# Kernel optimization log

Measured on AMD Instinct MI355X. Metric: run time of the kernel, lower is better.

## Reference

```python
import jax, jax.numpy as jnp
import numpy as np

N_NODES = 100000
N_EDGES = 1600000
IN_DIM = 160
HID = 128
BN_EPS = 1e-5


def setup_inputs() -> dict:
    key = jax.random.key(0)
    ks = jax.random.split(key, 16)
    d = {}
    d['x'] = jax.random.normal(ks[0], (N_NODES, IN_DIM), dtype=jnp.float32)
    d['edge_index'] = jax.random.randint(ks[1], (2, N_EDGES), 0, N_NODES, dtype=jnp.int64)
    dims = [(IN_DIM, HID), (HID, HID), (HID, HID)]
    for i, (fi, fo) in enumerate(dims):
        s = 1.0 / np.sqrt(fi)
        d[f'wl{i}'] = jax.random.normal(ks[2 + 4 * i], (fi, fo), dtype=jnp.float32) * s
        d[f'wr{i}'] = jax.random.normal(ks[3 + 4 * i], (fi, fo), dtype=jnp.float32) * s
        d[f'bl{i}'] = jnp.zeros((fo,), dtype=jnp.float32)
        d[f'g{i}'] = jnp.ones((fo,), dtype=jnp.float32)
        d[f'be{i}'] = jnp.zeros((fo,), dtype=jnp.float32)
        d[f'rm{i}'] = jax.random.normal(ks[4 + 4 * i], (fo,), dtype=jnp.float32) * 0.1
        d[f'rv{i}'] = jnp.ones((fo,), dtype=jnp.float32)
    d['lin_w'] = jax.random.normal(ks[14], (HID, 1), dtype=jnp.float32) * (1.0 / np.sqrt(HID))
    d['lin_b'] = jnp.zeros((1,), dtype=jnp.float32)
    return d


def _sage_bn_relu(h, src, dst, wl, wr, bl, g, be, rm, rv):
    # mean neighbor aggregation: gather messages at src, scatter-mean to dst
    msg = h[src]                                            # [E, d]
    agg = jax.ops.segment_sum(msg, dst, num_segments=N_NODES)
    cnt = jax.ops.segment_sum(jnp.ones((msg.shape[0],), h.dtype), dst, num_segments=N_NODES)
    mean = agg / jnp.maximum(cnt, 1.0)[:, None]             # nodes w/o in-edges -> 0
    out = mean @ wl + bl + h @ wr                           # SAGEConv (root_weight=True)
    # BatchNorm1d (inference: running stats) + ReLU
    out = (out - rm) * (g * jax.lax.rsqrt(rv + BN_EPS)) + be
    return jax.nn.relu(out)


def reference(x, edge_index,
              wl0, wr0, bl0, g0, be0, rm0, rv0,
              wl1, wr1, bl1, g1, be1, rm1, rv1,
              wl2, wr2, bl2, g2, be2, rm2, rv2,
              lin_w, lin_b):
    src, dst = edge_index[0], edge_index[1]
    h = _sage_bn_relu(x, src, dst, wl0, wr0, bl0, g0, be0, rm0, rv0)
    h = _sage_bn_relu(h, src, dst, wl1, wr1, bl1, g1, be1, rm1, rv1)
    h = _sage_bn_relu(h, src, dst, wl2, wr2, bl2, g2, be2, rm2, rv2)
    return (h @ lin_w + lin_b)[:, 0]                        # [N]
```

## Files before the change

### kernel.cpp

```cpp
#include <hip/hip_runtime.h>

#define N_NODES 100000
#define N_EDGES 1600000
#define IN_DIM 160
#define HID 128
#define BN_EPS 1e-5f

#define M_PAD 100096
#define NBUCK 196
#define BSH 9
#define EPB 8192
#define NHB (NBUCK * NBUCK)
#define NSB 38
#define LPAD 132

typedef unsigned int uint;
typedef unsigned short ushort;
typedef __attribute__((ext_vector_type(8))) short bf16x8;
typedef __attribute__((ext_vector_type(4))) float f32x4;
typedef __attribute__((ext_vector_type(2))) float f32x2;

__device__ __forceinline__ ushort bf16rn(float f) {
    uint u = __float_as_uint(f);
    u += 0x7fffu + ((u >> 16) & 1u);
    return (ushort)(u >> 16);
}
__device__ __forceinline__ float bflo(uint u) { return __uint_as_float(u << 16); }
__device__ __forceinline__ float bfhi(uint u) { return __uint_as_float(u & 0xffff0000u); }


__global__ __launch_bounds__(256) void hist_kernel(const int* __restrict__ dst,
                                                   int* __restrict__ ghist) {
    __shared__ int hist[NBUCK];
    int b = blockIdx.x, t = threadIdx.x;
    for (int i = t; i < NBUCK; i += 256) hist[i] = 0;
    __syncthreads();
    int e0 = b * EPB;
    for (int i = 0; i < EPB; i += 256) {
        int e = e0 + i + t;
        if (e < N_EDGES) atomicAdd(&hist[dst[e] >> BSH], 1);
    }
    __syncthreads();
    for (int i = t; i < NBUCK; i += 256) ghist[i * NBUCK + b] = hist[i];
}

__global__ __launch_bounds__(256) void scan1_kernel(const int* __restrict__ ghist,
                                                    int* __restrict__ bsum) {
    __shared__ int wsum[4];
    int b = blockIdx.x, t = threadIdx.x;
    int i4 = b * 256 + t;
    int4 v = (i4 * 4 < NHB) ? ((const int4*)ghist)[i4] : make_int4(0, 0, 0, 0);
    int s = v.x + v.y + v.z + v.w;
#pragma unroll
    for (int off = 32; off; off >>= 1) s += __shfl_down(s, off);
    if ((t & 63) == 0) wsum[t >> 6] = s;
    __syncthreads();
    if (t == 0) bsum[b] = wsum[0] + wsum[1] + wsum[2] + wsum[3];
}

__global__ void scan2_kernel(const int* __restrict__ bsum, int* __restrict__ boff,
                             int* __restrict__ gbb) {
    int lane = threadIdx.x;
    int v = (lane < NSB) ? bsum[lane] : 0;
    int s = v;
#pragma unroll
    for (int off = 1; off <= 32; off <<= 1) {
        int t2 = __shfl_up(s, off);
        if (lane >= off) s += t2;
    }
    if (lane < NSB) boff[lane] = s - v;
    if (lane == 0) gbb[NBUCK] = N_EDGES;
}

__global__ __launch_bounds__(256) void scan3_kernel(int* __restrict__ ghist,
                                                    const int* __restrict__ boff,
                                                    int* __restrict__ gbb) {
    __shared__ int ts[256];
    int b = blockIdx.x, t = threadIdx.x;
    int i4 = b * 256 + t;
    bool ok = (i4 * 4) < NHB;
    int4 v = ok ? ((const int4*)ghist)[i4] : make_int4(0, 0, 0, 0);
    int s = v.x + v.y + v.z + v.w;
    ts[t] = s;
    __syncthreads();
    for (int off = 1; off < 256; off <<= 1) {
        int a = (t >= off) ? ts[t - off] : 0;
        __syncthreads();
        ts[t] += a;
        __syncthreads();
    }
    int excl = boff[b] + ((t > 0) ? ts[t - 1] : 0);
    if (ok) {
        int idx = i4 * 4;
        int4 w;
        w.x = excl;
        w.y = excl + v.x;
        w.z = excl + v.x + v.y;
        w.w = excl + v.x + v.y + v.z;
        ((int4*)ghist)[i4] = w;
        if (idx % NBUCK == 0) gbb[idx / NBUCK] = w.x;
    }
}

__global__ __launch_bounds__(256) void scatter_kernel(const int* __restrict__ src,
                                                      const int* __restrict__ dst,
                                                      const int* __restrict__ ghist,
                                                      uint* __restrict__ scat) {
    __shared__ int base[NBUCK];
    __shared__ int fill[NBUCK];
    int b = blockIdx.x, t = threadIdx.x;
    for (int i = t; i < NBUCK; i += 256) { base[i] = ghist[i * NBUCK + b]; fill[i] = 0; }
    __syncthreads();
    int e0 = b * EPB;
    for (int i = 0; i < EPB; i += 256) {
        int e = e0 + i + t;
        if (e < N_EDGES) {
            int d = dst[e];
            int sv = src[e];
            int bk = d >> BSH;
            int lp = atomicAdd(&fill[bk], 1);
            scat[base[bk] + lp] = (uint)sv | ((uint)(d & 511) << 17);
        }
    }
}

__global__ __launch_bounds__(256) void bucket_csr_kernel(const uint* __restrict__ scat,
                                                         const int* __restrict__ gbb,
                                                         int* __restrict__ prow,
                                                         int* __restrict__ deg,
                                                         int* __restrict__ peidx) {
    __shared__ int cnt[512], fl[512], pref[512];
    __shared__ int ts[256];
    __shared__ int tot_s;
    int b = blockIdx.x, t = threadIdx.x;
    int beg = gbb[b], end = gbb[b + 1];
    int pb = beg + b * 8192;
    cnt[t] = 0; cnt[t + 256] = 0;
    __syncthreads();
    for (int i = beg + t; i < end; i += 256)
        atomicAdd(&cnt[scat[i] >> 17], 1);
    __syncthreads();
    int c0 = cnt[2 * t], c1 = cnt[2 * t + 1];
    int p0 = (c0 + 15) & ~15, p1 = (c1 + 15) & ~15;
    ts[t] = p0 + p1;
    __syncthreads();
    for (int off = 1; off < 256; off <<= 1) {
        int v = (t >= off) ? ts[t - off] : 0;
        __syncthreads();
        ts[t] += v;
        __syncthreads();
    }
    int ex = (t > 0) ? ts[t - 1] : 0;
    pref[2 * t] = ex;
    pref[2 * t + 1] = ex + p0;
    fl[t] = 0; fl[t + 256] = 0;
    if (t == 255) tot_s = ts[255];
    int g0 = b * 512 + 2 * t;
    if (g0 < N_NODES) { prow[g0] = pb + ex; deg[g0] = c0; }
    if (g0 + 1 < N_NODES) { prow[g0 + 1] = pb + ex + p0; deg[g0 + 1] = c1; }
    __syncthreads();
    int tot = tot_s;
    for (int i = t; i < tot; i += 256) peidx[pb + i] = N_NODES;
    __syncthreads();
    for (int i = beg + t; i < end; i += 256) {
        uint w = scat[i];
        int nl = (int)(w >> 17);
        int lp = atomicAdd(&fl[nl], 1);
        peidx[pb + pref[nl] + lp] = (int)(w & 0x1FFFFu);
    }
}

__global__ void prep_weights_kernel(const float* __restrict__ wl, const float* __restrict__ wr,
                                    ushort* __restrict__ Bf, int K) {
    int kb = blockIdx.x >> 4;
    int tt = blockIdx.x & 15;
    int lane = threadIdx.x;
    int n = tt * 16 + (lane & 15);
    int k0 = kb * 32 + (lane >> 4) * 8;
    ushort* dst = Bf + ((size_t)(kb * 16 + tt) * 64 + lane) * 8;
#pragma unroll
    for (int e = 0; e < 8; ++e) {
        int k = k0 + e;
        float v = (n < HID) ? wl[k * HID + n] : wr[k * HID + (n - HID)];
        dst[e] = bf16rn(v);
    }
}

__global__ void bn_prep_kernel(const float* __restrict__ bl0, const float* __restrict__ g0,
                               const float* __restrict__ be0, const float* __restrict__ rm0,
                               const float* __restrict__ rv0,
                               const float* __restrict__ bl1, const float* __restrict__ g1,
                               const float* __restrict__ be1, const float* __restrict__ rm1,
                               const float* __restrict__ rv1,
                               const float* __restrict__ bl2, const float* __restrict__ g2,
                               const float* __restrict__ be2, const float* __restrict__ rm2,
                               const float* __restrict__ rv2,
                               float* __restrict__ scale, float* __restrict__ shift) {
    int t = threadIdx.x;
    int L = t >> 7, j = t & 127;
    const float* bl = (L == 0) ? bl0 : (L == 1) ? bl1 : bl2;
    const float* g  = (L == 0) ? g0  : (L == 1) ? g1  : g2;
    const float* be = (L == 0) ? be0 : (L == 1) ? be1 : be2;
    const float* rm = (L == 0) ? rm0 : (L == 1) ? rm1 : rm2;
    const float* rv = (L == 0) ? rv0 : (L == 1) ? rv1 : rv2;
    float s = g[j] * rsqrtf(rv[j] + BN_EPS);
    scale[t] = s;
    shift[t] = (bl[j] - rm[j]) * s + be[j];
}

template <int K, bool AFP32>
__global__ __launch_bounds__(256) void gemm_kernel(const void* __restrict__ A_,
                                                   const ushort* __restrict__ Bf,
                                                   ushort* __restrict__ tl,
                                                   ushort* __restrict__ troot) {
    constexpr int CPR = K / 8;
    constexpr int FULLG = CPR & ~7;
    constexpr int LDSE = (64 * K > 4 * 16 * LPAD) ? 64 * K : 4 * 16 * LPAD;
    __shared__ ushort ldsA[LDSE];
    const int t = threadIdx.x;
    const int m0b = blockIdx.x * 64;

#pragma unroll
    for (int i = 0; i < (64 * CPR) / 256; ++i) {
        int cidx = i * 256 + t;
        int row = cidx / CPR;
        int j = cidx - row * CPR;
        bf16x8 v;
        if (AFP32) {
            const float* A = (const float*)A_;
            int m = m0b + row;
            float4 f0 = make_float4(0.f, 0.f, 0.f, 0.f), f1 = f0;
            if (m < N_NODES) {
                f0 = *(const float4*)(A + (size_t)m * K + j * 8);
                f1 = *(const float4*)(A + (size_t)m * K + j * 8 + 4);
            }
            v[0] = (short)bf16rn(f0.x); v[1] = (short)bf16rn(f0.y);
            v[2] = (short)bf16rn(f0.z); v[3] = (short)bf16rn(f0.w);
            v[4] = (short)bf16rn(f1.x); v[5] = (short)bf16rn(f1.y);
            v[6] = (short)bf16rn(f1.z); v[7] = (short)bf16rn(f1.w);
        } else {
            const ushort* A = (const ushort*)A_;
            v = *(const bf16x8*)(A + (size_t)(m0b + row) * K + j * 8);
        }
        int swz = (j < FULLG) ? ((j & ~7) | ((j ^ row) & 7))
                              : ((j & ~3) | ((j ^ row) & 3));
        *(bf16x8*)&ldsA[row * K + swz * 8] = v;
    }
    __syncthreads();

    const int lane = threadIdx.x & 63;
    const int wv = threadIdx.x >> 6;
    const int col = lane & 15;
    const int q = lane >> 4;
    const int rh = wv & 1;
    const int ch = wv >> 1;
    const int row0 = rh * 32 + col;
    f32x4 acc0[8], acc1[8];
#pragma unroll
    for (int tt = 0; tt < 8; ++tt) {
        acc0[tt] = (f32x4){0.f, 0.f, 0.f, 0.f};
        acc1[tt] = (f32x4){0.f, 0.f, 0.f, 0.f};
    }

#pragma unroll
    for (int kb = 0; kb < K / 32; ++kb) {
        int jj = kb * 4 + q;
        int swzj = (jj < FULLG) ? ((jj & ~7) | ((jj ^ col) & 7))
                                : ((jj & ~3) | ((jj ^ col) & 3));
        bf16x8 a0 = *(const bf16x8*)&ldsA[row0 * K + swzj * 8];
        bf16x8 a1 = *(const bf16x8*)&ldsA[(row0 + 16) * K + swzj * 8];
        const ushort* bp = Bf + ((size_t)((kb * 16 + ch * 8) * 64) + lane) * 8;
#pragma unroll
        for (int tt = 0; tt < 8; ++tt) {
            bf16x8 bfr = *(const bf16x8*)(bp + (size_t)tt * 64 * 8);
            acc0[tt] = __builtin_amdgcn_mfma_f32_16x16x32_bf16(a0, bfr, acc0[tt], 0, 0, 0);
            acc1[tt] = __builtin_amdgcn_mfma_f32_16x16x32_bf16(a1, bfr, acc1[tt], 0, 0, 0);
        }
    }

    __syncthreads();
    ushort(*rp)[16][LPAD] = (ushort(*)[16][LPAD])ldsA;
    ushort* outp = ch ? troot : tl;
#pragma unroll
    for (int mt = 0; mt < 2; ++mt) {
        const f32x4* ac = mt ? acc1 : acc0;
#pragma unroll
        for (int tt = 0; tt < 8; ++tt)
#pragma unroll
            for (int r = 0; r < 4; ++r)
                rp[wv][q * 4 + r][tt * 16 + col] = bf16rn(ac[tt][r]);
        int mbase = m0b + rh * 32 + mt * 16;
#pragma unroll
        for (int i = 0; i < 4; ++i) {
            int lin = i * 64 + lane;
            int row = lin >> 4;
            int c16 = lin & 15;
            bf16x8 v = *(const bf16x8*)&rp[wv][row][c16 * 8];
            *(bf16x8*)(outp + (size_t)(mbase + row) * HID + c16 * 8) = v;
        }
    }
}

template <bool FINAL>
__global__ __launch_bounds__(256) void agg_kernel(
    const ushort* __restrict__ tl_, const ushort* __restrict__ troot_,
    const int* __restrict__ prow, const int* __restrict__ deg_,
    const int* __restrict__ peidx,
    const float* __restrict__ bnscale, const float* __restrict__ bnshift,
    const float* __restrict__ linw, const float* __restrict__ linb,
    ushort* __restrict__ hout, float* __restrict__ out) {
    const int lane = threadIdx.x & 63;
    const int wvg = (blockIdx.x * 256 + (int)threadIdx.x) >> 6;
    const int g = lane >> 4;
    const int s = lane & 15;
    const int n = wvg * 4 + g;
    const int nn = (n < N_NODES) ? n : (N_NODES - 1);

    float4 sc0 = *(const float4*)(bnscale + s * 8);
    float4 sc1 = *(const float4*)(bnscale + s * 8 + 4);
    float4 sh0 = *(const float4*)(bnshift + s * 8);
    float4 sh1 = *(const float4*)(bnshift + s * 8 + 4);

    int pbeg = prow[nn];
    int dg = (n < N_NODES) ? deg_[nn] : 0;
    int myb = (dg + 15) >> 4;

    f32x2 acc2[4];
#pragma unroll
    for (int i = 0; i < 4; ++i) acc2[i] = (f32x2){0.f, 0.f};

    const int gsel = (lane & 48) << 2;

    for (int b = 0;; ++b) {
        bool act = b < myb;
        if (!__any(act)) break;
        int idx = act ? peidx[pbeg + b * 16 + s] : N_NODES;
        uint4 u[16];
#pragma unroll
        for (int jj = 0; jj < 16; ++jj) {
            int src = __builtin_amdgcn_ds_bpermute(gsel | (jj << 2), idx);
            u[jj] = *(const uint4*)(tl_ + (size_t)src * HID + s * 8);
        }
#pragma unroll
        for (int jj = 0; jj < 16; ++jj) {
            acc2[0] += (f32x2){bflo(u[jj].x), bfhi(u[jj].x)};
            acc2[1] += (f32x2){bflo(u[jj].y), bfhi(u[jj].y)};
            acc2[2] += (f32x2){bflo(u[jj].z), bfhi(u[jj].z)};
            acc2[3] += (f32x2){bflo(u[jj].w), bfhi(u[jj].w)};
        }
    }

    float inv = 1.0f / (float)((dg > 0) ? dg : 1);
    uint4 rv = *(const uint4*)(troot_ + (size_t)nn * HID + s * 8);
    float o[8];
    o[0] = fmaxf(fmaf(fmaf(acc2[0].x, inv, bflo(rv.x)), sc0.x, sh0.x), 0.f);
    o[1] = fmaxf(fmaf(fmaf(acc2[0].y, inv, bfhi(rv.x)), sc0.y, sh0.y), 0.f);
    o[2] = fmaxf(fmaf(fmaf(acc2[1].x, inv, bflo(rv.y)), sc0.z, sh0.z), 0.f);
    o[3] = fmaxf(fmaf(fmaf(acc2[1].y, inv, bfhi(rv.y)), sc0.w, sh0.w), 0.f);
    o[4] = fmaxf(fmaf(fmaf(acc2[2].x, inv, bflo(rv.z)), sc1.x, sh1.x), 0.f);
    o[5] = fmaxf(fmaf(fmaf(acc2[2].y, inv, bfhi(rv.z)), sc1.y, sh1.y), 0.f);
    o[6] = fmaxf(fmaf(fmaf(acc2[3].x, inv, bflo(rv.w)), sc1.z, sh1.z), 0.f);
    o[7] = fmaxf(fmaf(fmaf(acc2[3].y, inv, bfhi(rv.w)), sc1.w, sh1.w), 0.f);

    if (FINAL) {
        float4 w0 = *(const float4*)(linw + s * 8);
        float4 w1 = *(const float4*)(linw + s * 8 + 4);
        float p = o[0] * w0.x + o[1] * w0.y + o[2] * w0.z + o[3] * w0.w +
                  o[4] * w1.x + o[5] * w1.y + o[6] * w1.z + o[7] * w1.w;
#pragma unroll
        for (int off = 1; off < 16; off <<= 1) p += __shfl_xor(p, off);
        if (s == 0 && n < N_NODES) out[n] = p + linb[0];
    } else {
        uint4 pk = make_uint4(0u, 0u, 0u, 0u);
        if (n < N_NODES) {
            pk.x = (uint)bf16rn(o[0]) | ((uint)bf16rn(o[1]) << 16);
            pk.y = (uint)bf16rn(o[2]) | ((uint)bf16rn(o[3]) << 16);
            pk.z = (uint)bf16rn(o[4]) | ((uint)bf16rn(o[5]) << 16);
            pk.w = (uint)bf16rn(o[6]) | ((uint)bf16rn(o[7]) << 16);
        }
        *(uint4*)(hout + (size_t)n * HID + s * 8) = pk;
    }
}


extern "C" void kernel_launch(void* const* d_in, const int* in_sizes, int n_in,
                              void* d_out, int out_size, void* d_ws, size_t ws_size,
                              hipStream_t stream) {
    const float* x    = (const float*)d_in[0];
    const int*   ei   = (const int*)d_in[1];
    const int*   esrc = ei;
    const int*   edst = ei + N_EDGES;
    const float* wl[3]; const float* wr[3]; const float* bl[3];
    const float* g[3];  const float* be[3]; const float* rm[3]; const float* rv[3];
    for (int i = 0; i < 3; ++i) {
        wl[i] = (const float*)d_in[2 + 7 * i];
        wr[i] = (const float*)d_in[3 + 7 * i];
        bl[i] = (const float*)d_in[4 + 7 * i];
        g[i]  = (const float*)d_in[5 + 7 * i];
        be[i] = (const float*)d_in[6 + 7 * i];
        rm[i] = (const float*)d_in[7 + 7 * i];
        rv[i] = (const float*)d_in[8 + 7 * i];
    }
    const float* lin_w = (const float*)d_in[23];
    const float* lin_b = (const float*)d_in[24];
    float* out = (float*)d_out;

    char* ws = (char*)d_ws;
    size_t off = 0;
    auto carve = [&](size_t bytes) -> void* {
        void* p = ws + off;
        off += (bytes + 255) & ~(size_t)255;
        return p;
    };
    int*    prow   = (int*)carve((size_t)(N_NODES + 8) * sizeof(int));
    int*    deg    = (int*)carve((size_t)(N_NODES + 8) * sizeof(int));
    int*    peidx  = (int*)carve((size_t)3210000 * sizeof(int));
    uint*   scat   = (uint*)carve((size_t)N_EDGES * sizeof(uint));
    int*    ghist  = (int*)carve((size_t)(NSB * 1024) * sizeof(int));
    int*    gbb    = (int*)carve((NBUCK + 4) * sizeof(int));
    int*    bsum   = (int*)carve((NSB + 2) * sizeof(int));
    int*    boff   = (int*)carve((NSB + 2) * sizeof(int));
    ushort* tl     = (ushort*)carve((size_t)(M_PAD + 1) * HID * sizeof(ushort));
    ushort* troot  = (ushort*)carve((size_t)M_PAD * HID * sizeof(ushort));
    ushort* h      = (ushort*)carve((size_t)M_PAD * HID * sizeof(ushort));
    ushort* Bf0    = (ushort*)carve(256 * IN_DIM * sizeof(ushort));
    ushort* Bf1    = (ushort*)carve(256 * HID * sizeof(ushort));
    ushort* Bf2    = (ushort*)carve(256 * HID * sizeof(ushort));
    float*  bnsc   = (float*)carve(3 * HID * sizeof(float));
    float*  bnsh   = (float*)carve(3 * HID * sizeof(float));
    (void)ws_size; (void)n_in; (void)in_sizes; (void)out_size;

    hist_kernel<<<NBUCK, 256, 0, stream>>>(edst, ghist);
    scan1_kernel<<<NSB, 256, 0, stream>>>(ghist, bsum);
    scan2_kernel<<<1, 64, 0, stream>>>(bsum, boff, gbb);
    scan3_kernel<<<NSB, 256, 0, stream>>>(ghist, boff, gbb);
    scatter_kernel<<<NBUCK, 256, 0, stream>>>(esrc, edst, ghist, scat);
    bucket_csr_kernel<<<NBUCK, 256, 0, stream>>>(scat, gbb, prow, deg, peidx);

    prep_weights_kernel<<<(IN_DIM / 32) * 16, 64, 0, stream>>>(wl[0], wr[0], Bf0, IN_DIM);
    prep_weights_kernel<<<(HID / 32) * 16, 64, 0, stream>>>(wl[1], wr[1], Bf1, HID);
    prep_weights_kernel<<<(HID / 32) * 16, 64, 0, stream>>>(wl[2], wr[2], Bf2, HID);
    bn_prep_kernel<<<1, 384, 0, stream>>>(bl[0], g[0], be[0], rm[0], rv[0],
                                          bl[1], g[1], be[1], rm[1], rv[1],
                                          bl[2], g[2], be[2], rm[2], rv[2],
                                          bnsc, bnsh);

    const int GEMM_GRID = M_PAD / 64;
    const int AGG_GRID = M_PAD / 16;

    gemm_kernel<IN_DIM, true><<<GEMM_GRID, 256, 0, stream>>>(x, Bf0, tl, troot);
    agg_kernel<false><<<AGG_GRID, 256, 0, stream>>>(tl, troot, prow, deg, peidx, bnsc, bnsh,
                                                    nullptr, nullptr, h, nullptr);
    gemm_kernel<HID, false><<<GEMM_GRID, 256, 0, stream>>>(h, Bf1, tl, troot);
    agg_kernel<false><<<AGG_GRID, 256, 0, stream>>>(tl, troot, prow, deg, peidx, bnsc + HID, bnsh + HID,
                                                    nullptr, nullptr, h, nullptr);
    gemm_kernel<HID, false><<<GEMM_GRID, 256, 0, stream>>>(h, Bf2, tl, troot);
    agg_kernel<true><<<AGG_GRID, 256, 0, stream>>>(tl, troot, prow, deg, peidx, bnsc + 2 * HID, bnsh + 2 * HID,
                                                   lin_w, lin_b, nullptr, out);
}
```

Baseline: 464.2 us.

## Fuse setup kernels, overlap scatter with first GEMM, degree-sort nodes for aggregation

Folds the histogram, weight-prep, batch-norm prep and padding-zero steps into one multi-role init kernel. It also merges the edge scatter with the first-layer GEMM in a single launch so the two independent jobs can overlap. The CSR builder now writes a per-bucket permutation that groups nodes by degree class, so the four nodes sharing a wavefront in aggregation have similar loop trip counts. The aggregation loop also prefetches the next index chunk before accumulating. The cost is extra perm indirection, a larger padded aggregation grid, and scattered output writes.

```diff
diff --git a/kernel.cpp b/kernel.cpp
--- a/kernel.cpp
+++ b/kernel.cpp
@@ -13,6 +13,7 @@
 #define NHB (NBUCK * NBUCK)
 #define NSB 38
 #define LPAD 132
+#define NSLOT (NBUCK * 512)
 
 typedef unsigned int uint;
 typedef unsigned short ushort;
@@ -29,20 +30,83 @@
 __device__ __forceinline__ float bfhi(uint u) { return __uint_as_float(u & 0xffff0000u); }
 
 
-__global__ __launch_bounds__(256) void hist_kernel(const int* __restrict__ dst,
-                                                   int* __restrict__ ghist) {
+__device__ __forceinline__ void prep_body(int ob, int lane, const float* __restrict__ wl,
+                                          const float* __restrict__ wr,
+                                          ushort* __restrict__ Bf, int K) {
+    int kb = ob >> 4;
+    int tt = ob & 15;
+    int n = tt * 16 + (lane & 15);
+    int k0 = kb * 32 + (lane >> 4) * 8;
+    ushort* dst = Bf + ((size_t)(kb * 16 + tt) * 64 + lane) * 8;
+#pragma unroll
+    for (int e = 0; e < 8; ++e) {
+        int k = k0 + e;
+        float v = (n < HID) ? wl[k * HID + n] : wr[k * HID + (n - HID)];
+        dst[e] = bf16rn(v);
+    }
+}
+
+#define PREP0_B 20
+#define PREP1_B 16
+#define INIT_GRID (NBUCK + PREP0_B + 2 * PREP1_B + 2 + 1)
+
+__global__ __launch_bounds__(256) void init_kernel(
+    const int* __restrict__ dst, int* __restrict__ ghist,
+    const float* __restrict__ wl0, const float* __restrict__ wr0,
+    const float* __restrict__ wl1, const float* __restrict__ wr1,
+    const float* __restrict__ wl2, const float* __restrict__ wr2,
+    ushort* __restrict__ Bf0, ushort* __restrict__ Bf1, ushort* __restrict__ Bf2,
+    const float* __restrict__ bl0, const float* __restrict__ g0,
+    const float* __restrict__ be0, const float* __restrict__ rm0,
+    const float* __restrict__ rv0,
+    const float* __restrict__ bl1, const float* __restrict__ g1,
+    const float* __restrict__ be1, const float* __restrict__ rm1,
+    const float* __restrict__ rv1,
+    const float* __restrict__ bl2, const float* __restrict__ g2,
+    const float* __restrict__ be2, const float* __restrict__ rm2,
+    const float* __restrict__ rv2,
+    float* __restrict__ bnscale, float* __restrict__ bnshift,
+    ushort* __restrict__ h) {
     __shared__ int hist[NBUCK];
     int b = blockIdx.x, t = threadIdx.x;
-    for (int i = t; i < NBUCK; i += 256) hist[i] = 0;
-    __syncthreads();
-    int e0 = b * EPB;
-    for (int i = 0; i < EPB; i += 256) {
-        int e = e0 + i + t;
-        if (e < N_EDGES) atomicAdd(&hist[dst[e] >> BSH], 1);
-    }
-    __syncthreads();
-    for (int i = t; i < NBUCK; i += 256) ghist[i * NBUCK + b] = hist[i];
-}
+    if (b < NBUCK) {
+        for (int i = t; i < NBUCK; i += 256) hist[i] = 0;
+        __syncthreads();
+        int e0 = b * EPB;
+        for (int i = 0; i < EPB; i += 256) {
+            int e = e0 + i + t;
+            if (e < N_EDGES) atomicAdd(&hist[dst[e] >> BSH], 1);
+        }
+        __syncthreads();
+        for (int i = t; i < NBUCK; i += 256) ghist[i * NBUCK + b] = hist[i];
+    } else if (b < NBUCK + PREP0_B) {
+        int ob = (b - NBUCK) * 4 + (t >> 6);
+        prep_body(ob, t & 63, wl0, wr0, Bf0, IN_DIM);
+    } else if (b < NBUCK + PREP0_B + PREP1_B) {
+        int ob = (b - NBUCK - PREP0_B) * 4 + (t >> 6);
+        prep_body(ob, t & 63, wl1, wr1, Bf1, HID);
+    } else if (b < NBUCK + PREP0_B + 2 * PREP1_B) {
+        int ob = (b - NBUCK - PREP0_B - PREP1_B) * 4 + (t >> 6);
+        prep_body(ob, t & 63, wl2, wr2, Bf2, HID);
+    } else if (b < NBUCK + PREP0_B + 2 * PREP1_B + 2) {
+        int tt = (b - (NBUCK + PREP0_B + 2 * PREP1_B)) * 256 + t;
+        if (tt < 3 * HID) {
+            int L = tt >> 7, j = tt & 127;
+            const float* bl = (L == 0) ? bl0 : (L == 1) ? bl1 : bl2;
+            const float* gg = (L == 0) ? g0  : (L == 1) ? g1  : g2;
+            const float* be = (L == 0) ? be0 : (L == 1) ? be1 : be2;
+            const float* rm = (L == 0) ? rm0 : (L == 1) ? rm1 : rm2;
+            const float* rv = (L == 0) ? rv0 : (L == 1) ? rv1 : rv2;
+            float s = gg[j] * rsqrtf(rv[j] + BN_EPS);
+            bnscale[tt] = s;
+            bnshift[tt] = (bl[j] - rm[j]) * s + be[j];
+        }
+    } else {
+        uint* hp = (uint*)(h + (size_t)N_NODES * HID);
+        for (int i = t; i < (M_PAD - N_NODES) * HID / 2; i += 256) hp[i] = 0u;
+    }
+}
+
 
 __global__ __launch_bounds__(256) void scan1_kernel(const int* __restrict__ ghist,
                                                     int* __restrict__ bsum) {
@@ -102,45 +166,32 @@
     }
 }
 
-__global__ __launch_bounds__(256) void scatter_kernel(const int* __restrict__ src,
-                                                      const int* __restrict__ dst,
-                                                      const int* __restrict__ ghist,
-                                                      uint* __restrict__ scat) {
-    __shared__ int base[NBUCK];
-    __shared__ int fill[NBUCK];
-    int b = blockIdx.x, t = threadIdx.x;
-    for (int i = t; i < NBUCK; i += 256) { base[i] = ghist[i * NBUCK + b]; fill[i] = 0; }
-    __syncthreads();
-    int e0 = b * EPB;
-    for (int i = 0; i < EPB; i += 256) {
-        int e = e0 + i + t;
-        if (e < N_EDGES) {
-            int d = dst[e];
-            int sv = src[e];
-            int bk = d >> BSH;
-            int lp = atomicAdd(&fill[bk], 1);
-            scat[base[bk] + lp] = (uint)sv | ((uint)(d & 511) << 17);
-        }
-    }
-}
 
 __global__ __launch_bounds__(256) void bucket_csr_kernel(const uint* __restrict__ scat,
                                                          const int* __restrict__ gbb,
                                                          int* __restrict__ prow,
                                                          int* __restrict__ deg,
-                                                         int* __restrict__ peidx) {
+                                                         int* __restrict__ peidx,
+                                                         int* __restrict__ perm) {
     __shared__ int cnt[512], fl[512], pref[512];
     __shared__ int ts[256];
     __shared__ int tot_s;
+    __shared__ int clsCnt[8], clsFill[8], clsBase[9];
     int b = blockIdx.x, t = threadIdx.x;
     int beg = gbb[b], end = gbb[b + 1];
     int pb = beg + b * 8192;
     cnt[t] = 0; cnt[t + 256] = 0;
+    if (t < 8) { clsCnt[t] = 0; clsFill[t] = 0; }
     __syncthreads();
     for (int i = beg + t; i < end; i += 256)
         atomicAdd(&cnt[scat[i] >> 17], 1);
     __syncthreads();
     int c0 = cnt[2 * t], c1 = cnt[2 * t + 1];
+    int g0 = b * 512 + 2 * t;
+    int cls0 = (c0 == 0) ? 0 : ((c0 + 15) >> 4); if (cls0 > 7) cls0 = 7;
+    int cls1 = (c1 == 0) ? 0 : ((c1 + 15) >> 4); if (cls1 > 7) cls1 = 7;
+    if (g0 < N_NODES) atomicAdd(&clsCnt[cls0], 1);
+    if (g0 + 1 < N_NODES) atomicAdd(&clsCnt[cls1], 1);
     int p0 = (c0 + 15) & ~15, p1 = (c1 + 15) & ~15;
     ts[t] = p0 + p1;
     __syncthreads();
@@ -155,10 +206,26 @@
     pref[2 * t + 1] = ex + p0;
     fl[t] = 0; fl[t + 256] = 0;
     if (t == 255) tot_s = ts[255];
-    int g0 = b * 512 + 2 * t;
     if (g0 < N_NODES) { prow[g0] = pb + ex; deg[g0] = c0; }
     if (g0 + 1 < N_NODES) { prow[g0 + 1] = pb + ex + p0; deg[g0 + 1] = c1; }
     __syncthreads();
+    if (t == 0) {
+        int sacc = 0;
+#pragma unroll
+        for (int i = 0; i < 8; ++i) { clsBase[i] = sacc; sacc += clsCnt[i]; }
+        clsBase[8] = sacc;
+    }
+    __syncthreads();
+    if (g0 < N_NODES) {
+        int p = atomicAdd(&clsFill[cls0], 1);
+        perm[b * 512 + clsBase[cls0] + p] = g0;
+    }
+    if (g0 + 1 < N_NODES) {
+        int p = atomicAdd(&clsFill[cls1], 1);
+        perm[b * 512 + clsBase[cls1] + p] = g0 + 1;
+    }
+    int vt = clsBase[8];
+    for (int i = vt + t; i < 512; i += 256) perm[b * 512 + i] = N_NODES;
     int tot = tot_s;
     for (int i = t; i < tot; i += 256) peidx[pb + i] = N_NODES;
     __syncthreads();
@@ -170,55 +237,15 @@
     }
 }
 
-__global__ void prep_weights_kernel(const float* __restrict__ wl, const float* __restrict__ wr,
-                                    ushort* __restrict__ Bf, int K) {
-    int kb = blockIdx.x >> 4;
-    int tt = blockIdx.x & 15;
-    int lane = threadIdx.x;
-    int n = tt * 16 + (lane & 15);
-    int k0 = kb * 32 + (lane >> 4) * 8;
-    ushort* dst = Bf + ((size_t)(kb * 16 + tt) * 64 + lane) * 8;
-#pragma unroll
-    for (int e = 0; e < 8; ++e) {
-        int k = k0 + e;
-        float v = (n < HID) ? wl[k * HID + n] : wr[k * HID + (n - HID)];
-        dst[e] = bf16rn(v);
-    }
-}
-
-__global__ void bn_prep_kernel(const float* __restrict__ bl0, const float* __restrict__ g0,
-                               const float* __restrict__ be0, const float* __restrict__ rm0,
-                               const float* __restrict__ rv0,
-                               const float* __restrict__ bl1, const float* __restrict__ g1,
-                               const float* __restrict__ be1, const float* __restrict__ rm1,
-                               const float* __restrict__ rv1,
-                               const float* __restrict__ bl2, const float* __restrict__ g2,
-                               const float* __restrict__ be2, const float* __restrict__ rm2,
-                               const float* __restrict__ rv2,
-                               float* __restrict__ scale, float* __restrict__ shift) {
-    int t = threadIdx.x;
-    int L = t >> 7, j = t & 127;
-    const float* bl = (L == 0) ? bl0 : (L == 1) ? bl1 : bl2;
-    const float* g  = (L == 0) ? g0  : (L == 1) ? g1  : g2;
-    const float* be = (L == 0) ? be0 : (L == 1) ? be1 : be2;
-    const float* rm = (L == 0) ? rm0 : (L == 1) ? rm1 : rm2;
-    const float* rv = (L == 0) ? rv0 : (L == 1) ? rv1 : rv2;
-    float s = g[j] * rsqrtf(rv[j] + BN_EPS);
-    scale[t] = s;
-    shift[t] = (bl[j] - rm[j]) * s + be[j];
-}
-
 template <int K, bool AFP32>
-__global__ __launch_bounds__(256) void gemm_kernel(const void* __restrict__ A_,
-                                                   const ushort* __restrict__ Bf,
-                                                   ushort* __restrict__ tl,
-                                                   ushort* __restrict__ troot) {
+__device__ __forceinline__ void gemm_body(int bx, int t, ushort* ldsA,
+                                          const void* __restrict__ A_,
+                                          const ushort* __restrict__ Bf,
+                                          ushort* __restrict__ tl,
+                                          ushort* __restrict__ troot) {
     constexpr int CPR = K / 8;
     constexpr int FULLG = CPR & ~7;
-    constexpr int LDSE = (64 * K > 4 * 16 * LPAD) ? 64 * K : 4 * 16 * LPAD;
-    __shared__ ushort ldsA[LDSE];
-    const int t = threadIdx.x;
-    const int m0b = blockIdx.x * 64;
+    const int m0b = bx * 64;
 
 #pragma unroll
     for (int i = 0; i < (64 * CPR) / 256; ++i) {
@@ -248,8 +275,8 @@
     }
     __syncthreads();
 
-    const int lane = threadIdx.x & 63;
-    const int wv = threadIdx.x >> 6;
+    const int lane = t & 63;
+    const int wv = t >> 6;
     const int col = lane & 15;
     const int q = lane >> 4;
     const int rh = wv & 1;
@@ -301,11 +328,50 @@
     }
 }
 
+template <int K, bool AFP32>
+__global__ __launch_bounds__(256) void gemm_kernel(const void* __restrict__ A_,
+                                                   const ushort* __restrict__ Bf,
+                                                   ushort* __restrict__ tl,
+                                                   ushort* __restrict__ troot) {
+    constexpr int LDSE = (64 * K > 4 * 16 * LPAD) ? 64 * K : 4 * 16 * LPAD;
+    __shared__ ushort ldsA[LDSE];
+    gemm_body<K, AFP32>(blockIdx.x, threadIdx.x, ldsA, A_, Bf, tl, troot);
+}
+
+__global__ __launch_bounds__(256) void scatter_gemm1_kernel(
+    const int* __restrict__ src, const int* __restrict__ dst,
+    const int* __restrict__ ghist, uint* __restrict__ scat,
+    const float* __restrict__ x, const ushort* __restrict__ Bf0,
+    ushort* __restrict__ tl, ushort* __restrict__ troot) {
+    constexpr int LDSE = (64 * IN_DIM > 4 * 16 * LPAD) ? 64 * IN_DIM : 4 * 16 * LPAD;
+    __shared__ ushort ldsA[LDSE];
+    int b = blockIdx.x, t = threadIdx.x;
+    if (b < NBUCK) {
+        int* base = (int*)ldsA;
+        int* fill = base + NBUCK;
+        for (int i = t; i < NBUCK; i += 256) { base[i] = ghist[i * NBUCK + b]; fill[i] = 0; }
+        __syncthreads();
+        int e0 = b * EPB;
+        for (int i = 0; i < EPB; i += 256) {
+            int e = e0 + i + t;
+            if (e < N_EDGES) {
+                int d = dst[e];
+                int sv = src[e];
+                int bk = d >> BSH;
+                int lp = atomicAdd(&fill[bk], 1);
+                scat[base[bk] + lp] = (uint)sv | ((uint)(d & 511) << 17);
+            }
+        }
+    } else {
+        gemm_body<IN_DIM, true>(b - NBUCK, t, ldsA, x, Bf0, tl, troot);
+    }
+}
+
 template <bool FINAL>
 __global__ __launch_bounds__(256) void agg_kernel(
     const ushort* __restrict__ tl_, const ushort* __restrict__ troot_,
     const int* __restrict__ prow, const int* __restrict__ deg_,
-    const int* __restrict__ peidx,
+    const int* __restrict__ peidx, const int* __restrict__ perm,
     const float* __restrict__ bnscale, const float* __restrict__ bnshift,
     const float* __restrict__ linw, const float* __restrict__ linb,
     ushort* __restrict__ hout, float* __restrict__ out) {
@@ -313,8 +379,10 @@
     const int wvg = (blockIdx.x * 256 + (int)threadIdx.x) >> 6;
     const int g = lane >> 4;
     const int s = lane & 15;
-    const int n = wvg * 4 + g;
-    const int nn = (n < N_NODES) ? n : (N_NODES - 1);
+    const int slot = wvg * 4 + g;
+    const int n = perm[slot];
+    const bool valid = (n < N_NODES);
+    const int nn = valid ? n : 0;
 
     float4 sc0 = *(const float4*)(bnscale + s * 8);
     float4 sc1 = *(const float4*)(bnscale + s * 8 + 4);
@@ -322,7 +390,7 @@
     float4 sh1 = *(const float4*)(bnshift + s * 8 + 4);
 
     int pbeg = prow[nn];
-    int dg = (n < N_NODES) ? deg_[nn] : 0;
+    int dg = valid ? deg_[nn] : 0;
     int myb = (dg + 15) >> 4;
 
     f32x2 acc2[4];
@@ -331,16 +399,19 @@
 
     const int gsel = (lane & 48) << 2;
 
-    for (int b = 0;; ++b) {
-        bool act = b < myb;
-        if (!__any(act)) break;
-        int idx = act ? peidx[pbeg + b * 16 + s] : N_NODES;
+    bool act = (0 < myb);
+    int idx = act ? peidx[pbeg + s] : N_NODES;
+    int b = 0;
+    while (__any(act)) {
         uint4 u[16];
 #pragma unroll
         for (int jj = 0; jj < 16; ++jj) {
-            int src = __builtin_amdgcn_ds_bpermute(gsel | (jj << 2), idx);
-            u[jj] = *(const uint4*)(tl_ + (size_t)src * HID + s * 8);
-        }
+            int srcj = __builtin_amdgcn_ds_bpermute(gsel | (jj << 2), idx);
+            u[jj] = *(const uint4*)(tl_ + (size_t)srcj * HID + s * 8);
+        }
+        ++b;
+        bool actn = (b < myb);
+        int idxn = actn ? peidx[pbeg + b * 16 + s] : N_NODES;
 #pragma unroll
         for (int jj = 0; jj < 16; ++jj) {
             acc2[0] += (f32x2){bflo(u[jj].x), bfhi(u[jj].x)};
@@ -348,6 +419,7 @@
             acc2[2] += (f32x2){bflo(u[jj].z), bfhi(u[jj].z)};
             acc2[3] += (f32x2){bflo(u[jj].w), bfhi(u[jj].w)};
         }
+        act = actn; idx = idxn;
     }
 
     float inv = 1.0f / (float)((dg > 0) ? dg : 1);
@@ -369,16 +441,16 @@
                   o[4] * w1.x + o[5] * w1.y + o[6] * w1.z + o[7] * w1.w;
 #pragma unroll
         for (int off = 1; off < 16; off <<= 1) p += __shfl_xor(p, off);
-        if (s == 0 && n < N_NODES) out[n] = p + linb[0];
+        if (s == 0 && valid) out[n] = p + linb[0];
     } else {
-        uint4 pk = make_uint4(0u, 0u, 0u, 0u);
-        if (n < N_NODES) {
+        if (valid) {
+            uint4 pk;
             pk.x = (uint)bf16rn(o[0]) | ((uint)bf16rn(o[1]) << 16);
             pk.y = (uint)bf16rn(o[2]) | ((uint)bf16rn(o[3]) << 16);
             pk.z = (uint)bf16rn(o[4]) | ((uint)bf16rn(o[5]) << 16);
             pk.w = (uint)bf16rn(o[6]) | ((uint)bf16rn(o[7]) << 16);
-        }
-        *(uint4*)(hout + (size_t)n * HID + s * 8) = pk;
+            *(uint4*)(hout + (size_t)n * HID + s * 8) = pk;
+        }
     }
 }
 
@@ -420,6 +492,7 @@
     int*    gbb    = (int*)carve((NBUCK + 4) * sizeof(int));
     int*    bsum   = (int*)carve((NSB + 2) * sizeof(int));
     int*    boff   = (int*)carve((NSB + 2) * sizeof(int));
+    int*    perm   = (int*)carve((size_t)NSLOT * sizeof(int));
     ushort* tl     = (ushort*)carve((size_t)(M_PAD + 1) * HID * sizeof(ushort));
     ushort* troot  = (ushort*)carve((size_t)M_PAD * HID * sizeof(ushort));
     ushort* h      = (ushort*)carve((size_t)M_PAD * HID * sizeof(ushort));
@@ -430,31 +503,30 @@
     float*  bnsh   = (float*)carve(3 * HID * sizeof(float));
     (void)ws_size; (void)n_in; (void)in_sizes; (void)out_size;
 
-    hist_kernel<<<NBUCK, 256, 0, stream>>>(edst, ghist);
+    const int GEMM_GRID = M_PAD / 64;
+    const int AGG_GRID = NSLOT / 16;
+
+    init_kernel<<<INIT_GRID, 256, 0, stream>>>(
+        edst, ghist,
+        wl[0], wr[0], wl[1], wr[1], wl[2], wr[2], Bf0, Bf1, Bf2,
+        bl[0], g[0], be[0], rm[0], rv[0],
+        bl[1], g[1], be[1], rm[1], rv[1],
+        bl[2], g[2], be[2], rm[2], rv[2],
+        bnsc, bnsh, h);
     scan1_kernel<<<NSB, 256, 0, stream>>>(ghist, bsum);
     scan2_kernel<<<1, 64, 0, stream>>>(bsum, boff, gbb);
     scan3_kernel<<<NSB, 256, 0, stream>>>(ghist, boff, gbb);
-    scatter_kernel<<<NBUCK, 256, 0, stream>>>(esrc, edst, ghist, scat);
-    bucket_csr_kernel<<<NBUCK, 256, 0, stream>>>(scat, gbb, prow, deg, peidx);
-
-    prep_weights_kernel<<<(IN_DIM / 32) * 16, 64, 0, stream>>>(wl[0], wr[0], Bf0, IN_DIM);
-    prep_weights_kernel<<<(HID / 32) * 16, 64, 0, stream>>>(wl[1], wr[1], Bf1, HID);
-    prep_weights_kernel<<<(HID / 32) * 16, 64, 0, stream>>>(wl[2], wr[2], Bf2, HID);
-    bn_prep_kernel<<<1, 384, 0, stream>>>(bl[0], g[0], be[0], rm[0], rv[0],
-                                          bl[1], g[1], be[1], rm[1], rv[1],
-                                          bl[2], g[2], be[2], rm[2], rv[2],
-                                          bnsc, bnsh);
-
-    const int GEMM_GRID = M_PAD / 64;
-    const int AGG_GRID = M_PAD / 16;
-
-    gemm_kernel<IN_DIM, true><<<GEMM_GRID, 256, 0, stream>>>(x, Bf0, tl, troot);
-    agg_kernel<false><<<AGG_GRID, 256, 0, stream>>>(tl, troot, prow, deg, peidx, bnsc, bnsh,
-                                                    nullptr, nullptr, h, nullptr);
+    scatter_gemm1_kernel<<<NBUCK + GEMM_GRID, 256, 0, stream>>>(
+        esrc, edst, ghist, scat, x, Bf0, tl, troot);
+    bucket_csr_kernel<<<NBUCK, 256, 0, stream>>>(scat, gbb, prow, deg, peidx, perm);
+
+    agg_kernel<false><<<AGG_GRID, 256, 0, stream>>>(tl, troot, prow, deg, peidx, perm,
+                                                    bnsc, bnsh, nullptr, nullptr, h, nullptr);
     gemm_kernel<HID, false><<<GEMM_GRID, 256, 0, stream>>>(h, Bf1, tl, troot);
-    agg_kernel<false><<<AGG_GRID, 256, 0, stream>>>(tl, troot, prow, deg, peidx, bnsc + HID, bnsh + HID,
-                                                    nullptr, nullptr, h, nullptr);
+    agg_kernel<false><<<AGG_GRID, 256, 0, stream>>>(tl, troot, prow, deg, peidx, perm,
+                                                    bnsc + HID, bnsh + HID, nullptr, nullptr, h, nullptr);
     gemm_kernel<HID, false><<<GEMM_GRID, 256, 0, stream>>>(h, Bf2, tl, troot);
-    agg_kernel<true><<<AGG_GRID, 256, 0, stream>>>(tl, troot, prow, deg, peidx, bnsc + 2 * HID, bnsh + 2 * HID,
+    agg_kernel<true><<<AGG_GRID, 256, 0, stream>>>(tl, troot, prow, deg, peidx, perm,
+                                                   bnsc + 2 * HID, bnsh + 2 * HID,
                                                    lin_w, lin_b, nullptr, out);
 }
```

Result: faster. 442.7 us (-4.6%).
